# Kernel tuning notes

Measured on AMD Instinct MI355X. Metric: run time of the kernel, lower is better.

Reference implementation:

```python
import jax, jax.numpy as jnp
import numpy as np

B = 4096
INPUT_SIZE = 256
LATENT = 64
HIDDEN = 512
ACTIONS = 12
EXPERTS = 8
GATE_H = 128
IN_DIM = INPUT_SIZE + LATENT      # 320, first-layer expert in-dim
INTER = HIDDEN + LATENT           # 576, later-layer expert in-dim


def _lip_linear_params(key, out_f, in_f):
    kw, kb = jax.random.split(key)
    stdv = 1.0 / np.sqrt(in_f)
    W = jax.random.uniform(kw, (out_f, in_f), jnp.float32, -stdv, stdv)
    b = jax.random.uniform(kb, (out_f,), jnp.float32, -stdv, stdv)
    c = jnp.abs(W).sum(1).max()[None]  # shape (1,), matches init
    return W, b, c


def _expert_params(key, e, in_f, out_f):
    # kaiming_uniform_ on tensor of shape (E, in, out): fan_in computed by torch
    kw = key
    gain = np.sqrt(2.0)  # default a=sqrt(5) -> gain = sqrt(2/(1+5)) ... torch uses a=math.sqrt(5)? no: default a=0
    # torch.nn.init.kaiming_uniform_(weight) default a=0, fan_in = in*out? torch computes fan from dims[1:]
    fan_in = in_f
    bound = np.sqrt(6.0 / fan_in)
    W = jax.random.uniform(kw, (e, in_f, out_f), jnp.float32, -bound, bound)
    b = jnp.full((e, out_f), 0.01, jnp.float32)
    return W, b


def setup_inputs() -> dict:
    key = jax.random.key(0)
    ks = jax.random.split(key, 10)
    z = jax.random.normal(ks[0], (B, LATENT), jnp.float32)
    c = jax.random.normal(ks[1], (B, INPUT_SIZE), jnp.float32)
    w0, b0 = _expert_params(ks[2], EXPERTS, IN_DIM, HIDDEN)
    w1, b1 = _expert_params(ks[3], EXPERTS, INTER, HIDDEN)
    w2, b2 = _expert_params(ks[4], EXPERTS, INTER, ACTIONS)
    gw0, gb0, gc0 = _lip_linear_params(ks[5], GATE_H, IN_DIM)
    gw1, gb1, gc1 = _lip_linear_params(ks[6], GATE_H, GATE_H)
    gw2, gb2, gc2 = _lip_linear_params(ks[7], EXPERTS, GATE_H)
    return {"z": z, "c": c, "w0": w0, "b0": b0, "w1": w1, "b1": b1,
            "w2": w2, "b2": b2, "gw0": gw0, "gb0": gb0, "gc0": gc0,
            "gw1": gw1, "gb1": gb1, "gc1": gc1, "gw2": gw2, "gb2": gb2, "gc2": gc2}


def _lip_linear(x, W, b, cc):
    # LipschitzLinear: scale rows of W so row-wise L1 norm <= softplus(c)
    lipc = jax.nn.softplus(cc)                      # (1,)
    scale = jnp.minimum(lipc / jnp.abs(W).sum(1), 1.0)  # (out,)
    return x @ (W * scale[:, None]).T + b


def _moe_forward(z, c, coeff, layers):
    layer_out = c
    for W, bias, act in layers:
        inp = jnp.concatenate([z, layer_out], axis=1)       # (B, in)
        # per-expert GEMM then coefficient mix: avoids (B,in,out) intermediate
        h = jnp.einsum('bi,eio->beo', inp, W)               # (B, E, out)
        out = jnp.einsum('be,beo->bo', coeff, h) + coeff @ bias
        layer_out = jax.nn.elu(out) if act else out
    return layer_out


def reference(z, c, w0, b0, w1, b1, w2, b2,
              gw0, gb0, gc0, gw1, gb1, gc1, gw2, gb2, gc2):
    x = jnp.concatenate([z, c], axis=1)
    h = jax.nn.elu(_lip_linear(x, gw0, gb0, gc0))
    h = jax.nn.elu(_lip_linear(h, gw1, gb1, gc1))
    logits = _lip_linear(h, gw2, gb2, gc2)
    coeff = jax.nn.softmax(logits, axis=1)                  # (B, E)
    layers = [(w0, b0, True), (w1, b1, True), (w2, b2, False)]
    return _moe_forward(z, c, coeff, layers)
```

## Files before the change

kernel.cpp:

```cpp
#include <hip/hip_runtime.h>
#include <hip/hip_bf16.h>
#include <hip/hip_fp16.h>
#include <math.h>

#define BATCH 4096
#define INPUT_SIZE 256
#define LATENT 64
#define HIDDEN 512
#define ACTIONS 12
#define EXPERTS 8
#define GATE_H 128
#define IN_DIM (INPUT_SIZE + LATENT)
#define INTER (HIDDEN + LATENT)

typedef unsigned int u32;
typedef unsigned short u16;
typedef __attribute__((ext_vector_type(8))) short short8;
typedef __attribute__((ext_vector_type(8))) _Float16 f16x8;
typedef __attribute__((ext_vector_type(16))) float f32x16;

__device__ __forceinline__ u16 f2h(float x) { return __half_as_ushort(__float2half(x)); }
__device__ __forceinline__ float h2f(u16 u) { return __half2float(__ushort_as_half(u)); }

__device__ __forceinline__ void gload16(const void* g, void* lds) {
    __builtin_amdgcn_global_load_lds(
        (const __attribute__((address_space(1))) u32*)g,
        (__attribute__((address_space(3))) u32*)lds, 16, 0, 0);
}

__global__ void scale_all_kernel(
    const float* __restrict__ gw0, const float* __restrict__ gc0, float* __restrict__ W0t,
    const float* __restrict__ gw1, const float* __restrict__ gc1, float* __restrict__ W1t,
    const float* __restrict__ gw2, const float* __restrict__ gc2, float* __restrict__ W2t) {
    const int bid = blockIdx.x;
    const float* W; const float* cc; float* Wt; int cols, rows, row;
    if (bid < 128)      { W = gw0; cc = gc0; Wt = W0t; cols = IN_DIM; rows = GATE_H; row = bid; }
    else if (bid < 256) { W = gw1; cc = gc1; Wt = W1t; cols = GATE_H; rows = GATE_H; row = bid - 128; }
    else                { W = gw2; cc = gc2; Wt = W2t; cols = GATE_H; rows = EXPERTS; row = bid - 256; }
    const float* w = W + (size_t)row * cols;
    float s = 0.f;
    for (int i = threadIdx.x; i < cols; i += 64) s += fabsf(w[i]);
    #pragma unroll
    for (int off = 32; off > 0; off >>= 1) s += __shfl_down(s, off, 64);
    s = __shfl(s, 0, 64);
    const float cv = cc[0];
    const float lipc = (cv > 0.f) ? (cv + log1pf(expf(-cv))) : log1pf(expf(cv));
    const float scale = fminf(lipc / s, 1.0f);
    for (int i = threadIdx.x; i < cols; i += 64)
        Wt[(size_t)i * rows + row] = w[i] * scale;
}

#define GS 4
__global__ __launch_bounds__(256) void gate_forward_v4(
    const float* __restrict__ z, const float* __restrict__ c,
    const float* __restrict__ W0t, const float* __restrict__ b0,
    const float* __restrict__ W1t, const float* __restrict__ b1,
    const float* __restrict__ W2t, const float* __restrict__ b2,
    float* __restrict__ coeff) {
    __shared__ float xs[GS][IN_DIM + 2];
    __shared__ float hq[4][GS][GATE_H];
    __shared__ float h1[GS][GATE_H + 1];
    __shared__ float h2[GS][GATE_H + 1];
    __shared__ float red[GS][EXPERTS];

    const int b4 = blockIdx.x * GS;
    const int t = threadIdx.x;
    const int np = t & 63, kq = t >> 6;
    const int n0 = np * 2;

    for (int idx = t; idx < GS * IN_DIM; idx += 256) {
        const int s = idx / IN_DIM, i = idx - s * IN_DIM;
        xs[s][i] = (i < LATENT) ? z[(size_t)(b4 + s) * LATENT + i]
                                : c[(size_t)(b4 + s) * INPUT_SIZE + (i - LATENT)];
    }
    __syncthreads();

    {
        float a0[GS], a1[GS];
        #pragma unroll
        for (int s = 0; s < GS; ++s) { a0[s] = 0.f; a1[s] = 0.f; }
        const int i0 = kq * 80;
        #pragma unroll 8
        for (int i = i0; i < i0 + 80; ++i) {
            const float2 wv = *(const float2*)(W0t + (size_t)i * GATE_H + n0);
            #pragma unroll
            for (int s = 0; s < GS; ++s) {
                a0[s] = fmaf(xs[s][i], wv.x, a0[s]);
                a1[s] = fmaf(xs[s][i], wv.y, a1[s]);
            }
        }
        #pragma unroll
        for (int s = 0; s < GS; ++s) { hq[kq][s][n0] = a0[s]; hq[kq][s][n0 + 1] = a1[s]; }
    }
    __syncthreads();
    if (kq == 0) {
        #pragma unroll
        for (int s = 0; s < GS; ++s)
            #pragma unroll
            for (int j = 0; j < 2; ++j) {
                const int n = n0 + j;
                const float v = b0[n] + hq[0][s][n] + hq[1][s][n] + hq[2][s][n] + hq[3][s][n];
                h1[s][n] = v > 0.f ? v : expm1f(v);
            }
    }
    __syncthreads();

    {
        float a0[GS], a1[GS];
        #pragma unroll
        for (int s = 0; s < GS; ++s) { a0[s] = 0.f; a1[s] = 0.f; }
        const int i0 = kq * 32;
        #pragma unroll 8
        for (int i = i0; i < i0 + 32; ++i) {
            const float2 wv = *(const float2*)(W1t + (size_t)i * GATE_H + n0);
            #pragma unroll
            for (int s = 0; s < GS; ++s) {
                a0[s] = fmaf(h1[s][i], wv.x, a0[s]);
                a1[s] = fmaf(h1[s][i], wv.y, a1[s]);
            }
        }
        #pragma unroll
        for (int s = 0; s < GS; ++s) { hq[kq][s][n0] = a0[s]; hq[kq][s][n0 + 1] = a1[s]; }
    }
    __syncthreads();
    if (kq == 0) {
        #pragma unroll
        for (int s = 0; s < GS; ++s)
            #pragma unroll
            for (int j = 0; j < 2; ++j) {
                const int n = n0 + j;
                const float v = b1[n] + hq[0][s][n] + hq[1][s][n] + hq[2][s][n] + hq[3][s][n];
                h2[s][n] = v > 0.f ? v : expm1f(v);
            }
    }
    __syncthreads();

    if (t < GS * EXPERTS) {
        const int s = t >> 3, e = t & 7;
        float acc = b2[e];
        #pragma unroll 8
        for (int i = 0; i < GATE_H; ++i)
            acc = fmaf(h2[s][i], W2t[(size_t)i * EXPERTS + e], acc);
        red[s][e] = acc;
    }
    __syncthreads();
    if (t < GS) {
        float m = red[t][0];
        #pragma unroll
        for (int i = 1; i < EXPERTS; ++i) m = fmaxf(m, red[t][i]);
        float e[EXPERTS];
        float sum = 0.f;
        #pragma unroll
        for (int i = 0; i < EXPERTS; ++i) { e[i] = expf(red[t][i] - m); sum += e[i]; }
        const float inv = 1.f / sum;
        #pragma unroll
        for (int i = 0; i < EXPERTS; ++i)
            coeff[(size_t)(b4 + t) * EXPERTS + i] = e[i] * inv;
    }
}

__global__ __launch_bounds__(256) void pack_all_kernel(
    const float* __restrict__ w0, const float* __restrict__ w1,
    const float* __restrict__ w2,
    const float* __restrict__ z, const float* __restrict__ c,
    u16* __restrict__ Bpk0, u16* __restrict__ Bpk1, u16* __restrict__ Bpk2,
    u16* __restrict__ Apk0, u16* __restrict__ Apk1, u16* __restrict__ Apk2) {
    const int t = threadIdx.x, wv = t >> 6, l = t & 63;
    const int x = blockIdx.x, y = blockIdx.y;

    if (y < 33) {
        __shared__ float tile[4][16][33];
        const float* w; u16* Bpk; int IN, OUT, nblk;
        if (y < 16)      { w = w0; Bpk = Bpk0; IN = IN_DIM; OUT = HIDDEN;  nblk = y; }
        else if (y < 32) { w = w1; Bpk = Bpk1; IN = INTER;  OUT = HIDDEN;  nblk = y - 16; }
        else             { w = w2; Bpk = Bpk2; IN = INTER;  OUT = ACTIONS; nblk = 0; }
        const int NK = IN / 16;
        const int e = x, n0 = nblk * 32;
        const int col = l & 31, half = l >> 5;
        char* base = (char*)Bpk + ((size_t)(nblk * EXPERTS + e) * NK) * 1024;

        for (int jj = wv; jj < NK; jj += 4) {
            #pragma unroll
            for (int i = 0; i < 8; ++i) {
                const int r = i * 2 + half;
                float v = 0.f;
                if (n0 + col < OUT) v = w[((size_t)e * IN + jj * 16 + r) * OUT + n0 + col];
                tile[wv][r][col] = v;
            }
            short8 hh;
            #pragma unroll
            for (int i = 0; i < 8; ++i)
                hh[i] = (short)f2h(tile[wv][half * 8 + i][col]);
            *(short8*)(base + (size_t)jj * 1024 + l * 16) = hh;
        }
    } else {
        constexpr int NK0 = 20, NK1 = 36;
        const int bblk = (y - 33) * 8 + x;
        const int r = l & 31, half = l >> 5;
        const int row = bblk * 32 + r;
        char* base0 = (char*)Apk0 + (size_t)bblk * NK0 * 1024;
        char* base1 = (char*)Apk1 + (size_t)bblk * NK1 * 1024;
        char* base2 = (char*)Apk2 + (size_t)bblk * NK1 * 1024;

        for (int jj = wv; jj < NK0; jj += 4) {
            const int k = jj * 16 + half * 8;
            const float* src = (k < LATENT) ? (z + (size_t)row * LATENT + k)
                                            : (c + (size_t)row * INPUT_SIZE + (k - LATENT));
            short8 hh;
            #pragma unroll
            for (int i = 0; i < 8; ++i) hh[i] = (short)f2h(src[i]);
            *(short8*)(base0 + (size_t)jj * 1024 + l * 16) = hh;
            if (jj < 4) {
                *(short8*)(base1 + (size_t)jj * 1024 + l * 16) = hh;
                *(short8*)(base2 + (size_t)jj * 1024 + l * 16) = hh;
            }
        }
    }
}

template<int NPART>
__global__ __launch_bounds__(256) void reduce_pack_kernel(
    const float* __restrict__ P, const float* __restrict__ coeff,
    const float* __restrict__ bias, u16* __restrict__ ApkNext) {
    constexpr int NK = 36;
    __shared__ float biasS[EXPERTS][256];
    __shared__ float coeffS[32][9];
    const int t = threadIdx.x, wv = t >> 6, l = t & 63;
    const int bblk = blockIdx.x, ch = blockIdx.y;
    const int r = l & 31, half = l >> 5;
    const int row = bblk * 32 + r;

    for (int idx = t; idx < EXPERTS * 256; idx += 256)
        biasS[idx >> 8][idx & 255] = bias[(idx >> 8) * HIDDEN + ch * 256 + (idx & 255)];
    for (int idx = t; idx < 32 * 8; idx += 256)
        coeffS[idx >> 3][idx & 7] = coeff[(size_t)(bblk * 32 + (idx >> 3)) * 8 + (idx & 7)];
    __syncthreads();

    char* base = (char*)ApkNext + (size_t)bblk * NK * 1024;
    for (int jj = ch * 16 + wv; jj < ch * 16 + 16; jj += 4) {
        const int cb = jj * 16 + half * 8;
        float v[8];
        #pragma unroll
        for (int i = 0; i < 8; ++i) v[i] = 0.f;
        #pragma unroll
        for (int p = 0; p < NPART; ++p) {
            const float4* q = (const float4*)(P + ((size_t)p * BATCH + row) * HIDDEN + cb);
            const float4 a = q[0], b = q[1];
            v[0] += a.x; v[1] += a.y; v[2] += a.z; v[3] += a.w;
            v[4] += b.x; v[5] += b.y; v[6] += b.z; v[7] += b.w;
        }
        #pragma unroll
        for (int e = 0; e < EXPERTS; ++e) {
            const float cv = coeffS[r][e];
            #pragma unroll
            for (int i = 0; i < 8; ++i) v[i] = fmaf(cv, biasS[e][cb - ch * 256 + i], v[i]);
        }
        short8 hh;
        #pragma unroll
        for (int i = 0; i < 8; ++i) {
            const float hv = v[i] > 0.f ? v[i] : expm1f(v[i]);
            hh[i] = (short)f2h(hv);
        }
        *(short8*)(base + (size_t)(4 + jj) * 1024 + l * 16) = hh;
    }
}

__global__ __launch_bounds__(256) void reduce_out_kernel(
    const float* __restrict__ P2, const float* __restrict__ coeff,
    const float* __restrict__ b2, float* __restrict__ out) {
    const int t = threadIdx.x;
    const int bblk = blockIdx.x;
    for (int idx = t; idx < 32 * ACTIONS; idx += 256) {
        const int r = idx / ACTIONS, n = idx % ACTIONS;
        const int row = bblk * 32 + r;
        float s = 0.f;
        #pragma unroll
        for (int p = 0; p < 8; ++p) s += P2[((size_t)p * BATCH + row) * 32 + n];
        const float* cf = coeff + (size_t)row * 8;
        #pragma unroll
        for (int e = 0; e < 8; ++e) s = fmaf(cf[e], b2[e * ACTIONS + n], s);
        out[(size_t)row * ACTIONS + n] = s;
    }
}

template<int NK, int WN, int EPB, int OUTW, int GX, int GY, int GZ>
__global__ __launch_bounds__(128 * WN) void moe_gemm(
    const u16* __restrict__ Apk, const u16* __restrict__ Bpk,
    const float* __restrict__ coeff, float* __restrict__ P) {
    constexpr int TOT = NK / 4;
    constexpr int NWAVE = 2 * WN;
    constexpr int CPW = 16 / NWAVE;
    constexpr int CPX = GX / 8;

    __shared__ __align__(16) char As[3 * 16384];
    __shared__ float coeffT[EPB][128];

    const int t = threadIdx.x, wv = t >> 6, l = t & 63;
    const int wr = wv & 1, wc = wv >> 1;

    const int fid = blockIdx.x + GX * (blockIdx.y + GY * blockIdx.z);
    const int xcd = fid & 7, idx = fid >> 3;
    const int bx = xcd * CPX + (idx % CPX);
    const int yz = idx / CPX;
    const int by = yz % GY, bz = yz / GY;

    const int b0 = bx * 128;
    const int bblk0 = bx * 4;
    const int nblkg = by * WN + wc;
    const int part = bz;
    const int estart = part * EPB;

    for (int idx2 = t; idx2 < EPB * 128; idx2 += 128 * WN)
        coeffT[idx2 >> 7][idx2 & 127] =
            coeff[(size_t)(b0 + (idx2 & 127)) * EXPERTS + estart + (idx2 >> 7)];

    const char* Ab = (const char*)Apk;
    const char* Bbase[EPB];
    #pragma unroll
    for (int e = 0; e < EPB; ++e)
        Bbase[e] = (const char*)Bpk +
                   ((size_t)(nblkg * EXPERTS + estart + e) * NK) * 1024 + l * 16;

    f32x16 accE[EPB][2];
    #pragma unroll
    for (int e = 0; e < EPB; ++e) { accE[e][0] = (f32x16)0.f; accE[e][1] = (f32x16)0.f; }

    f16x8 breg[2][EPB][4];

    auto stageA = [&](int s) {
        char* dst = As + (s % 3) * 16384;
        #pragma unroll
        for (int q = 0; q < CPW; ++q) {
            const int cf = wv * CPW + q, bb = cf >> 2, kq = cf & 3;
            gload16(Ab + ((size_t)(bblk0 + bb) * NK + s * 4 + kq) * 1024 + l * 16,
                    dst + cf * 1024 + l * 16);
        }
    };

    __syncthreads();

    stageA(0);
    #pragma unroll
    for (int e = 0; e < EPB; ++e)
        #pragma unroll
        for (int q = 0; q < 4; ++q)
            breg[0][e][q] = *(const f16x8*)(Bbase[e] + (size_t)q * 1024);
    stageA(1);
    #pragma unroll
    for (int e = 0; e < EPB; ++e)
        #pragma unroll
        for (int q = 0; q < 4; ++q)
            breg[1][e][q] = *(const f16x8*)(Bbase[e] + (size_t)(4 + q) * 1024);

    #pragma unroll
    for (int s = 0; s < TOT; ++s) {
        if (s == TOT - 1) asm volatile("s_waitcnt vmcnt(0)" ::: "memory");
        else              asm volatile("s_waitcnt vmcnt(12)" ::: "memory");
        __builtin_amdgcn_sched_barrier(0);
        __builtin_amdgcn_s_barrier();
        __builtin_amdgcn_sched_barrier(0);

        if (s + 2 < TOT) stageA(s + 2);

        const char* buf = As + (s % 3) * 16384;
        f16x8 af0[4], af1[4];
        #pragma unroll
        for (int j = 0; j < 4; ++j) {
            af0[j] = *(const f16x8*)(buf + ((wr * 2 + 0) * 4 + j) * 1024 + l * 16);
            af1[j] = *(const f16x8*)(buf + ((wr * 2 + 1) * 4 + j) * 1024 + l * 16);
        }
        #pragma unroll
        for (int e = 0; e < EPB; ++e)
            #pragma unroll
            for (int j = 0; j < 4; ++j) {
                accE[e][0] = __builtin_amdgcn_mfma_f32_32x32x16_f16(af0[j], breg[s & 1][e][j], accE[e][0], 0, 0, 0);
                accE[e][1] = __builtin_amdgcn_mfma_f32_32x32x16_f16(af1[j], breg[s & 1][e][j], accE[e][1], 0, 0, 0);
            }
        if (s + 2 < TOT) {
            #pragma unroll
            for (int e = 0; e < EPB; ++e)
                #pragma unroll
                for (int q = 0; q < 4; ++q)
                    breg[s & 1][e][q] = *(const f16x8*)(Bbase[e] + (size_t)((s + 2) * 4 + q) * 1024);
        }
    }

    const int ncol = nblkg * 32 + (l & 31);
    #pragma unroll
    for (int m = 0; m < 2; ++m) {
        #pragma unroll
        for (int g = 0; g < 16; ++g) {
            const int rloc = (g & 3) + 8 * (g >> 2) + 4 * (l >> 5);
            const int row = wr * 64 + m * 32 + rloc;
            float v = 0.f;
            #pragma unroll
            for (int e = 0; e < EPB; ++e) v = fmaf(coeffT[e][row], accE[e][m][g], v);
            P[((size_t)part * BATCH + b0 + row) * OUTW + ncol] = v;
        }
    }
}

extern "C" void kernel_launch(void* const* d_in, const int* in_sizes, int n_in,
                              void* d_out, int out_size, void* d_ws, size_t ws_size,
                              hipStream_t stream) {
    const float* z   = (const float*)d_in[0];
    const float* c   = (const float*)d_in[1];
    const float* w0  = (const float*)d_in[2];
    const float* b0  = (const float*)d_in[3];
    const float* w1  = (const float*)d_in[4];
    const float* b1  = (const float*)d_in[5];
    const float* w2  = (const float*)d_in[6];
    const float* b2  = (const float*)d_in[7];
    const float* gw0 = (const float*)d_in[8];
    const float* gb0 = (const float*)d_in[9];
    const float* gc0 = (const float*)d_in[10];
    const float* gw1 = (const float*)d_in[11];
    const float* gb1 = (const float*)d_in[12];
    const float* gc1 = (const float*)d_in[13];
    const float* gw2 = (const float*)d_in[14];
    const float* gb2 = (const float*)d_in[15];
    const float* gc2 = (const float*)d_in[16];
    float* out = (float*)d_out;

    char* p = (char*)d_ws;
    float* coeff = (float*)p;  p += (size_t)BATCH * EXPERTS * 4;
    float* gW0t  = (float*)p;  p += (size_t)GATE_H * IN_DIM * 4;
    float* gW1t  = (float*)p;  p += (size_t)GATE_H * GATE_H * 4;
    float* gW2t  = (float*)p;  p += (size_t)EXPERTS * GATE_H * 4;
    u16* Apk0 = (u16*)p;       p += (size_t)128 * 20 * 1024;
    u16* Apk1 = (u16*)p;       p += (size_t)128 * 36 * 1024;
    u16* Apk2 = (u16*)p;       p += (size_t)128 * 36 * 1024;
    u16* Bpk0 = (u16*)p;       p += (size_t)16 * 8 * 20 * 1024;
    u16* Bpk1 = (u16*)p;       p += (size_t)16 * 8 * 36 * 1024;
    u16* Bpk2 = (u16*)p;       p += (size_t)8 * 36 * 1024;
    float* P  = (float*)p;     p += (size_t)4 * BATCH * HIDDEN * 4;

    scale_all_kernel<<<264, 64, 0, stream>>>(gw0, gc0, gW0t, gw1, gc1, gW1t,
                                             gw2, gc2, gW2t);
    gate_forward_v4<<<BATCH / GS, 256, 0, stream>>>(z, c, gW0t, gb0, gW1t, gb1,
                                                    gW2t, gb2, coeff);

    pack_all_kernel<<<dim3(8, 49), 256, 0, stream>>>(w0, w1, w2, z, c,
                                                     Bpk0, Bpk1, Bpk2,
                                                     Apk0, Apk1, Apk2);

    moe_gemm<20, 2, 2, HIDDEN, 32, 8, 4><<<dim3(32, 8, 4), 256, 0, stream>>>(
        Apk0, Bpk0, coeff, P);
    reduce_pack_kernel<4><<<dim3(128, 2), 256, 0, stream>>>(P, coeff, b0, Apk1);

    moe_gemm<36, 2, 2, HIDDEN, 32, 8, 4><<<dim3(32, 8, 4), 256, 0, stream>>>(
        Apk1, Bpk1, coeff, P);
    reduce_pack_kernel<4><<<dim3(128, 2), 256, 0, stream>>>(P, coeff, b1, Apk2);

    moe_gemm<36, 1, 1, 32, 32, 1, 8><<<dim3(32, 1, 8), 128, 0, stream>>>(
        Apk2, Bpk2, coeff, P);
    reduce_out_kernel<<<128, 256, 0, stream>>>(P, coeff, b2, out);
}
```

Before: 120.9 us.

## Fuse expert GEMM with coefficient reduce, bias, ELU and repack per block

```diff
diff --git a/kernel.cpp b/kernel.cpp
--- a/kernel.cpp
+++ b/kernel.cpp
@@ -218,53 +218,6 @@
     }
 }
 
-template<int NPART>
-__global__ __launch_bounds__(256) void reduce_pack_kernel(
-    const float* __restrict__ P, const float* __restrict__ coeff,
-    const float* __restrict__ bias, u16* __restrict__ ApkNext) {
-    constexpr int NK = 36;
-    __shared__ float biasS[EXPERTS][256];
-    __shared__ float coeffS[32][9];
-    const int t = threadIdx.x, wv = t >> 6, l = t & 63;
-    const int bblk = blockIdx.x, ch = blockIdx.y;
-    const int r = l & 31, half = l >> 5;
-    const int row = bblk * 32 + r;
-
-    for (int idx = t; idx < EXPERTS * 256; idx += 256)
-        biasS[idx >> 8][idx & 255] = bias[(idx >> 8) * HIDDEN + ch * 256 + (idx & 255)];
-    for (int idx = t; idx < 32 * 8; idx += 256)
-        coeffS[idx >> 3][idx & 7] = coeff[(size_t)(bblk * 32 + (idx >> 3)) * 8 + (idx & 7)];
-    __syncthreads();
-
-    char* base = (char*)ApkNext + (size_t)bblk * NK * 1024;
-    for (int jj = ch * 16 + wv; jj < ch * 16 + 16; jj += 4) {
-        const int cb = jj * 16 + half * 8;
-        float v[8];
-        #pragma unroll
-        for (int i = 0; i < 8; ++i) v[i] = 0.f;
-        #pragma unroll
-        for (int p = 0; p < NPART; ++p) {
-            const float4* q = (const float4*)(P + ((size_t)p * BATCH + row) * HIDDEN + cb);
-            const float4 a = q[0], b = q[1];
-            v[0] += a.x; v[1] += a.y; v[2] += a.z; v[3] += a.w;
-            v[4] += b.x; v[5] += b.y; v[6] += b.z; v[7] += b.w;
-        }
-        #pragma unroll
-        for (int e = 0; e < EXPERTS; ++e) {
-            const float cv = coeffS[r][e];
-            #pragma unroll
-            for (int i = 0; i < 8; ++i) v[i] = fmaf(cv, biasS[e][cb - ch * 256 + i], v[i]);
-        }
-        short8 hh;
-        #pragma unroll
-        for (int i = 0; i < 8; ++i) {
-            const float hv = v[i] > 0.f ? v[i] : expm1f(v[i]);
-            hh[i] = (short)f2h(hv);
-        }
-        *(short8*)(base + (size_t)(4 + jj) * 1024 + l * 16) = hh;
-    }
-}
-
 __global__ __launch_bounds__(256) void reduce_out_kernel(
     const float* __restrict__ P2, const float* __restrict__ coeff,
     const float* __restrict__ b2, float* __restrict__ out) {
@@ -280,6 +233,137 @@
         #pragma unroll
         for (int e = 0; e < 8; ++e) s = fmaf(cf[e], b2[e * ACTIONS + n], s);
         out[(size_t)row * ACTIONS + n] = s;
+    }
+}
+
+template<int NK>
+__global__ __launch_bounds__(256) void moe_gemm_fused(
+    const u16* __restrict__ Apk, const u16* __restrict__ Bpk,
+    const float* __restrict__ coeff, const float* __restrict__ bias,
+    u16* __restrict__ ApkNext) {
+    constexpr int TOT = NK / 4;
+    constexpr int GTOT = 8 * TOT;
+    constexpr int NKN = 36;
+
+    __shared__ __align__(16) char As[3 * 16384];
+    __shared__ float coeffT[EXPERTS][128];
+    __shared__ float biasS[EXPERTS][64];
+
+    const int t = threadIdx.x, wv = t >> 6, l = t & 63;
+    const int wr = wv & 1, wc = wv >> 1;
+
+    const int fid = blockIdx.x + 32 * blockIdx.y;
+    const int xcd = fid & 7, idx = fid >> 3;
+    const int bx = xcd * 4 + (idx & 3);
+    const int by = idx >> 2;
+
+    const int b0 = bx * 128;
+    const int bblk0 = bx * 4;
+    const int n0 = by * 64;
+    const int nblkg = by * 2 + wc;
+
+    for (int i2 = t; i2 < EXPERTS * 128; i2 += 256)
+        coeffT[i2 >> 7][i2 & 127] = coeff[(size_t)(b0 + (i2 & 127)) * EXPERTS + (i2 >> 7)];
+    for (int i2 = t; i2 < EXPERTS * 64; i2 += 256)
+        biasS[i2 >> 6][i2 & 63] = bias[(i2 >> 6) * HIDDEN + n0 + (i2 & 63)];
+
+    const char* Ab = (const char*)Apk;
+    const char* Bb = (const char*)Bpk + ((size_t)nblkg * EXPERTS * NK) * 1024 + l * 16;
+
+    f32x16 accF[2], accE[2];
+    accF[0] = (f32x16)0.f; accF[1] = (f32x16)0.f;
+    accE[0] = (f32x16)0.f; accE[1] = (f32x16)0.f;
+
+    f16x8 breg[2][4];
+
+    auto stageA = [&](int g2) {
+        const int s2 = g2 % TOT;
+        char* dst = As + (g2 % 3) * 16384;
+        #pragma unroll
+        for (int q = 0; q < 4; ++q) {
+            const int cf = wv * 4 + q, bb = cf >> 2, kq = cf & 3;
+            gload16(Ab + ((size_t)(bblk0 + bb) * NK + s2 * 4 + kq) * 1024 + l * 16,
+                    dst + cf * 1024 + l * 16);
+        }
+    };
+    auto bload = [&](int g2, int set) {
+        const int e2 = g2 / TOT, ks = g2 % TOT;
+        #pragma unroll
+        for (int q = 0; q < 4; ++q)
+            breg[set][q] = *(const f16x8*)(Bb + (size_t)(e2 * NK + ks * 4 + q) * 1024);
+    };
+
+    __syncthreads();
+
+    stageA(0); bload(0, 0);
+    stageA(1); bload(1, 1);
+
+    #pragma unroll
+    for (int g = 0; g < GTOT; ++g) {
+        if (g == GTOT - 1) asm volatile("s_waitcnt vmcnt(0)" ::: "memory");
+        else               asm volatile("s_waitcnt vmcnt(8)" ::: "memory");
+        __builtin_amdgcn_sched_barrier(0);
+        __builtin_amdgcn_s_barrier();
+        __builtin_amdgcn_sched_barrier(0);
+
+        if (g + 2 < GTOT) stageA(g + 2);
+
+        const char* buf = As + (g % 3) * 16384;
+        f16x8 af0[4], af1[4];
+        #pragma unroll
+        for (int j = 0; j < 4; ++j) {
+            af0[j] = *(const f16x8*)(buf + ((wr * 2 + 0) * 4 + j) * 1024 + l * 16);
+            af1[j] = *(const f16x8*)(buf + ((wr * 2 + 1) * 4 + j) * 1024 + l * 16);
+        }
+        #pragma unroll
+        for (int j = 0; j < 4; ++j) {
+            accE[0] = __builtin_amdgcn_mfma_f32_32x32x16_f16(af0[j], breg[g & 1][j], accE[0], 0, 0, 0);
+            accE[1] = __builtin_amdgcn_mfma_f32_32x32x16_f16(af1[j], breg[g & 1][j], accE[1], 0, 0, 0);
+        }
+        if (g + 2 < GTOT) bload(g + 2, g & 1);
+
+        if ((g + 1) % TOT == 0) {
+            const int e = g / TOT;
+            #pragma unroll
+            for (int m = 0; m < 2; ++m) {
+                #pragma unroll
+                for (int i = 0; i < 16; ++i) {
+                    const int row = wr * 64 + m * 32 + (i & 3) + 8 * (i >> 2) + 4 * (l >> 5);
+                    accF[m][i] = fmaf(coeffT[e][row], accE[m][i], accF[m][i]);
+                    accE[m][i] = 0.f;
+                }
+            }
+        }
+    }
+
+    __syncthreads();
+    u16* Cs = (u16*)As;
+    const int cl = wc * 32 + (l & 31);
+    #pragma unroll
+    for (int m = 0; m < 2; ++m) {
+        #pragma unroll
+        for (int i = 0; i < 16; ++i) {
+            const int rl = wr * 64 + m * 32 + (i & 3) + 8 * (i >> 2) + 4 * (l >> 5);
+            float bm = 0.f;
+            #pragma unroll
+            for (int e = 0; e < EXPERTS; ++e)
+                bm = fmaf(coeffT[e][rl], biasS[e][cl], bm);
+            float v = accF[m][i] + bm;
+            v = v > 0.f ? v : expm1f(v);
+            Cs[rl * 72 + cl] = f2h(v);
+        }
+    }
+    __syncthreads();
+
+    const int jjbase = 4 + by * 4;
+    #pragma unroll
+    for (int q = 0; q < 4; ++q) {
+        const int cch = wv * 4 + q, bb = cch >> 2, jj = cch & 3;
+        const int row = bb * 32 + (l & 31);
+        const int colb = jj * 16 + (l >> 5) * 8;
+        const short8 val = *(const short8*)(Cs + row * 72 + colb);
+        *(short8*)((char*)ApkNext +
+                   ((size_t)(bblk0 + bb) * NKN + jjbase + jj) * 1024 + l * 16) = val;
     }
 }
 
@@ -433,7 +517,7 @@
     u16* Bpk0 = (u16*)p;       p += (size_t)16 * 8 * 20 * 1024;
     u16* Bpk1 = (u16*)p;       p += (size_t)16 * 8 * 36 * 1024;
     u16* Bpk2 = (u16*)p;       p += (size_t)8 * 36 * 1024;
-    float* P  = (float*)p;     p += (size_t)4 * BATCH * HIDDEN * 4;
+    float* P  = (float*)p;     p += (size_t)8 * BATCH * 32 * 4;
 
     scale_all_kernel<<<264, 64, 0, stream>>>(gw0, gc0, gW0t, gw1, gc1, gW1t,
                                              gw2, gc2, gW2t);
@@ -444,13 +528,9 @@
                                                      Bpk0, Bpk1, Bpk2,
                                                      Apk0, Apk1, Apk2);
 
-    moe_gemm<20, 2, 2, HIDDEN, 32, 8, 4><<<dim3(32, 8, 4), 256, 0, stream>>>(
-        Apk0, Bpk0, coeff, P);
-    reduce_pack_kernel<4><<<dim3(128, 2), 256, 0, stream>>>(P, coeff, b0, Apk1);
-
-    moe_gemm<36, 2, 2, HIDDEN, 32, 8, 4><<<dim3(32, 8, 4), 256, 0, stream>>>(
-        Apk1, Bpk1, coeff, P);
-    reduce_pack_kernel<4><<<dim3(128, 2), 256, 0, stream>>>(P, coeff, b1, Apk2);
+    moe_gemm_fused<20><<<dim3(32, 8), 256, 0, stream>>>(Apk0, Bpk0, coeff, b0, Apk1);
+
+    moe_gemm_fused<36><<<dim3(32, 8), 256, 0, stream>>>(Apk1, Bpk1, coeff, b1, Apk2);
 
     moe_gemm<36, 1, 1, 32, 32, 1, 8><<<dim3(32, 1, 8), 128, 0, stream>>>(
         Apk2, Bpk2, coeff, P);
```

Result: slower. 136.8 us (+13.2%).

## Store GEMM partial sums in fp16 and fold gate scaling into pack kernel

Applied to the files above, without the earlier changes.

```diff
diff --git a/kernel.cpp b/kernel.cpp
--- a/kernel.cpp
+++ b/kernel.cpp
@@ -26,28 +26,6 @@
     __builtin_amdgcn_global_load_lds(
         (const __attribute__((address_space(1))) u32*)g,
         (__attribute__((address_space(3))) u32*)lds, 16, 0, 0);
-}
-
-__global__ void scale_all_kernel(
-    const float* __restrict__ gw0, const float* __restrict__ gc0, float* __restrict__ W0t,
-    const float* __restrict__ gw1, const float* __restrict__ gc1, float* __restrict__ W1t,
-    const float* __restrict__ gw2, const float* __restrict__ gc2, float* __restrict__ W2t) {
-    const int bid = blockIdx.x;
-    const float* W; const float* cc; float* Wt; int cols, rows, row;
-    if (bid < 128)      { W = gw0; cc = gc0; Wt = W0t; cols = IN_DIM; rows = GATE_H; row = bid; }
-    else if (bid < 256) { W = gw1; cc = gc1; Wt = W1t; cols = GATE_H; rows = GATE_H; row = bid - 128; }
-    else                { W = gw2; cc = gc2; Wt = W2t; cols = GATE_H; rows = EXPERTS; row = bid - 256; }
-    const float* w = W + (size_t)row * cols;
-    float s = 0.f;
-    for (int i = threadIdx.x; i < cols; i += 64) s += fabsf(w[i]);
-    #pragma unroll
-    for (int off = 32; off > 0; off >>= 1) s += __shfl_down(s, off, 64);
-    s = __shfl(s, 0, 64);
-    const float cv = cc[0];
-    const float lipc = (cv > 0.f) ? (cv + log1pf(expf(-cv))) : log1pf(expf(cv));
-    const float scale = fminf(lipc / s, 1.0f);
-    for (int i = threadIdx.x; i < cols; i += 64)
-        Wt[(size_t)i * rows + row] = w[i] * scale;
 }
 
 #define GS 4
@@ -82,11 +60,11 @@
         const int i0 = kq * 80;
         #pragma unroll 8
         for (int i = i0; i < i0 + 80; ++i) {
-            const float2 wv = *(const float2*)(W0t + (size_t)i * GATE_H + n0);
+            const float2 wv2 = *(const float2*)(W0t + (size_t)i * GATE_H + n0);
             #pragma unroll
             for (int s = 0; s < GS; ++s) {
-                a0[s] = fmaf(xs[s][i], wv.x, a0[s]);
-                a1[s] = fmaf(xs[s][i], wv.y, a1[s]);
+                a0[s] = fmaf(xs[s][i], wv2.x, a0[s]);
+                a1[s] = fmaf(xs[s][i], wv2.y, a1[s]);
             }
         }
         #pragma unroll
@@ -112,11 +90,11 @@
         const int i0 = kq * 32;
         #pragma unroll 8
         for (int i = i0; i < i0 + 32; ++i) {
-            const float2 wv = *(const float2*)(W1t + (size_t)i * GATE_H + n0);
+            const float2 wv2 = *(const float2*)(W1t + (size_t)i * GATE_H + n0);
             #pragma unroll
             for (int s = 0; s < GS; ++s) {
-                a0[s] = fmaf(h1[s][i], wv.x, a0[s]);
-                a1[s] = fmaf(h1[s][i], wv.y, a1[s]);
+                a0[s] = fmaf(h1[s][i], wv2.x, a0[s]);
+                a1[s] = fmaf(h1[s][i], wv2.y, a1[s]);
             }
         }
         #pragma unroll
@@ -164,7 +142,11 @@
     const float* __restrict__ w2,
     const float* __restrict__ z, const float* __restrict__ c,
     u16* __restrict__ Bpk0, u16* __restrict__ Bpk1, u16* __restrict__ Bpk2,
-    u16* __restrict__ Apk0, u16* __restrict__ Apk1, u16* __restrict__ Apk2) {
+    u16* __restrict__ Apk0, u16* __restrict__ Apk1, u16* __restrict__ Apk2,
+    const float* __restrict__ gw0, const float* __restrict__ gc0,
+    const float* __restrict__ gw1, const float* __restrict__ gc1,
+    const float* __restrict__ gw2, const float* __restrict__ gc2,
+    float* __restrict__ gW0t, float* __restrict__ gW1t, float* __restrict__ gW2t) {
     const int t = threadIdx.x, wv = t >> 6, l = t & 63;
     const int x = blockIdx.x, y = blockIdx.y;
 
@@ -193,7 +175,7 @@
                 hh[i] = (short)f2h(tile[wv][half * 8 + i][col]);
             *(short8*)(base + (size_t)jj * 1024 + l * 16) = hh;
         }
-    } else {
+    } else if (y < 49) {
         constexpr int NK0 = 20, NK1 = 36;
         const int bblk = (y - 33) * 8 + x;
         const int r = l & 31, half = l >> 5;
@@ -215,12 +197,31 @@
                 *(short8*)(base2 + (size_t)jj * 1024 + l * 16) = hh;
             }
         }
+    } else {
+        const int row_g = (y - 49) * 32 + x * 4 + wv;
+        if (row_g < 264) {
+            const float* W; const float* cc; float* Wt; int cols, rows, row;
+            if (row_g < 128)      { W = gw0; cc = gc0; Wt = gW0t; cols = IN_DIM; rows = GATE_H; row = row_g; }
+            else if (row_g < 256) { W = gw1; cc = gc1; Wt = gW1t; cols = GATE_H; rows = GATE_H; row = row_g - 128; }
+            else                  { W = gw2; cc = gc2; Wt = gW2t; cols = GATE_H; rows = EXPERTS; row = row_g - 256; }
+            const float* w = W + (size_t)row * cols;
+            float s = 0.f;
+            for (int i = l; i < cols; i += 64) s += fabsf(w[i]);
+            #pragma unroll
+            for (int off = 32; off > 0; off >>= 1) s += __shfl_down(s, off, 64);
+            s = __shfl(s, 0, 64);
+            const float cv = cc[0];
+            const float lipc = (cv > 0.f) ? (cv + log1pf(expf(-cv))) : log1pf(expf(cv));
+            const float scale = fminf(lipc / s, 1.0f);
+            for (int i = l; i < cols; i += 64)
+                Wt[(size_t)i * rows + row] = w[i] * scale;
+        }
     }
 }
 
 template<int NPART>
 __global__ __launch_bounds__(256) void reduce_pack_kernel(
-    const float* __restrict__ P, const float* __restrict__ coeff,
+    const u16* __restrict__ P16, const float* __restrict__ coeff,
     const float* __restrict__ bias, u16* __restrict__ ApkNext) {
     constexpr int NK = 36;
     __shared__ float biasS[EXPERTS][256];
@@ -244,10 +245,9 @@
         for (int i = 0; i < 8; ++i) v[i] = 0.f;
         #pragma unroll
         for (int p = 0; p < NPART; ++p) {
-            const float4* q = (const float4*)(P + ((size_t)p * BATCH + row) * HIDDEN + cb);
-            const float4 a = q[0], b = q[1];
-            v[0] += a.x; v[1] += a.y; v[2] += a.z; v[3] += a.w;
-            v[4] += b.x; v[5] += b.y; v[6] += b.z; v[7] += b.w;
+            const short8 q = *(const short8*)(P16 + ((size_t)p * BATCH + row) * HIDDEN + cb);
+            #pragma unroll
+            for (int i = 0; i < 8; ++i) v[i] += h2f((u16)q[i]);
         }
         #pragma unroll
         for (int e = 0; e < EXPERTS; ++e) {
@@ -283,10 +283,10 @@
     }
 }
 
-template<int NK, int WN, int EPB, int OUTW, int GX, int GY, int GZ>
+template<int NK, int WN, int EPB, int OUTW, int GX, int GY, int GZ, bool F16P>
 __global__ __launch_bounds__(128 * WN) void moe_gemm(
     const u16* __restrict__ Apk, const u16* __restrict__ Bpk,
-    const float* __restrict__ coeff, float* __restrict__ P) {
+    const float* __restrict__ coeff, void* __restrict__ Pout) {
     constexpr int TOT = NK / 4;
     constexpr int NWAVE = 2 * WN;
     constexpr int CPW = 16 / NWAVE;
@@ -395,7 +395,9 @@
             float v = 0.f;
             #pragma unroll
             for (int e = 0; e < EPB; ++e) v = fmaf(coeffT[e][row], accE[e][m][g], v);
-            P[((size_t)part * BATCH + b0 + row) * OUTW + ncol] = v;
+            const size_t off = ((size_t)part * BATCH + b0 + row) * OUTW + ncol;
+            if (F16P) ((u16*)Pout)[off] = f2h(v);
+            else      ((float*)Pout)[off] = v;
         }
     }
 }
@@ -433,26 +435,25 @@
     u16* Bpk0 = (u16*)p;       p += (size_t)16 * 8 * 20 * 1024;
     u16* Bpk1 = (u16*)p;       p += (size_t)16 * 8 * 36 * 1024;
     u16* Bpk2 = (u16*)p;       p += (size_t)8 * 36 * 1024;
-    float* P  = (float*)p;     p += (size_t)4 * BATCH * HIDDEN * 4;
-
-    scale_all_kernel<<<264, 64, 0, stream>>>(gw0, gc0, gW0t, gw1, gc1, gW1t,
-                                             gw2, gc2, gW2t);
+    u16* P16  = (u16*)p;       p += (size_t)4 * BATCH * HIDDEN * 2;
+    float* P32 = (float*)P16;
+
+    pack_all_kernel<<<dim3(8, 58), 256, 0, stream>>>(
+        w0, w1, w2, z, c, Bpk0, Bpk1, Bpk2, Apk0, Apk1, Apk2,
+        gw0, gc0, gw1, gc1, gw2, gc2, gW0t, gW1t, gW2t);
+
     gate_forward_v4<<<BATCH / GS, 256, 0, stream>>>(z, c, gW0t, gb0, gW1t, gb1,
                                                     gW2t, gb2, coeff);
 
-    pack_all_kernel<<<dim3(8, 49), 256, 0, stream>>>(w0, w1, w2, z, c,
-                                                     Bpk0, Bpk1, Bpk2,
-                                                     Apk0, Apk1, Apk2);
-
-    moe_gemm<20, 2, 2, HIDDEN, 32, 8, 4><<<dim3(32, 8, 4), 256, 0, stream>>>(
-        Apk0, Bpk0, coeff, P);
-    reduce_pack_kernel<4><<<dim3(128, 2), 256, 0, stream>>>(P, coeff, b0, Apk1);
-
-    moe_gemm<36, 2, 2, HIDDEN, 32, 8, 4><<<dim3(32, 8, 4), 256, 0, stream>>>(
-        Apk1, Bpk1, coeff, P);
-    reduce_pack_kernel<4><<<dim3(128, 2), 256, 0, stream>>>(P, coeff, b1, Apk2);
-
-    moe_gemm<36, 1, 1, 32, 32, 1, 8><<<dim3(32, 1, 8), 128, 0, stream>>>(
-        Apk2, Bpk2, coeff, P);
-    reduce_out_kernel<<<128, 256, 0, stream>>>(P, coeff, b2, out);
-}
+    moe_gemm<20, 2, 2, HIDDEN, 32, 8, 4, true><<<dim3(32, 8, 4), 256, 0, stream>>>(
+        Apk0, Bpk0, coeff, P16);
+    reduce_pack_kernel<4><<<dim3(128, 2), 256, 0, stream>>>(P16, coeff, b0, Apk1);
+
+    moe_gemm<36, 2, 2, HIDDEN, 32, 8, 4, true><<<dim3(32, 8, 4), 256, 0, stream>>>(
+        Apk1, Bpk1, coeff, P16);
+    reduce_pack_kernel<4><<<dim3(128, 2), 256, 0, stream>>>(P16, coeff, b1, Apk2);
+
+    moe_gemm<36, 1, 1, 32, 32, 1, 8, false><<<dim3(32, 1, 8), 128, 0, stream>>>(
+        Apk2, Bpk2, coeff, P32);
+    reduce_out_kernel<<<128, 256, 0, stream>>>(P32, coeff, b2, out);
+}
```

New measurement: 116.0 us (median of 2 runs). -4.1%, faster.
